# Performance work log

Hardware: AMD Instinct MI355X
Metric: run time of the kernel (lower is better)

## Reference

```python
import jax, jax.numpy as jnp
import numpy as np

LODS = [16, 32, 64, 128, 256]
SCENE_SCALE = 4.0
DESC = 4
N = 2_000_000
# 8 corner offsets of a voxel, bit-decoded: (x, y, z) in {0,1}^3
_CORNERS = jnp.asarray([[(i >> 2) & 1, (i >> 1) & 1, i & 1] for i in range(8)], dtype=jnp.int32)  # (8,3)


def setup_inputs() -> dict:
    key = jax.random.key(0)
    ks = jax.random.split(key, 2 + len(LODS))
    inp = {
        "pts": jax.random.normal(ks[0], (N, 3), dtype=jnp.float32),
        "d": jax.random.normal(ks[1], (N, 3), dtype=jnp.float32),
    }
    # codebook init mirrors torch: zeros + 0.01 * randn, shape (LOD^3, desc)
    for i, res in enumerate(LODS):
        inp[f"codebook_{i}"] = jax.random.normal(ks[2 + i], (res ** 3, DESC), dtype=jnp.float32) * 0.01
    return inp


def _trilerp(res, codebook, pts01):
    """NGLOD-style dense-grid trilinear interpolation.
    pts01: (N,3) in [0,1]; codebook: (res^3, DESC). Returns (N, DESC)."""
    pos = pts01 * (res - 1)                                   # (N,3) in [0, res-1]
    c0 = jnp.clip(jnp.floor(pos).astype(jnp.int32), 0, res - 2)
    frac = pos - c0.astype(pos.dtype)                         # (N,3) in [0,1]
    idx = c0[:, None, :] + _CORNERS[None, :, :]               # (N,8,3)
    flat = (idx[..., 0] * res + idx[..., 1]) * res + idx[..., 2]  # (N,8) row-major x*res^2+y*res+z
    # trilinear weights: prod over axes of (frac if corner bit set else 1-frac)
    w = jnp.prod(jnp.where(_CORNERS[None] == 1, frac[:, None, :], 1.0 - frac[:, None, :]), axis=-1)  # (N,8)
    return jnp.einsum('nkd,nk->nd', codebook[flat], w)        # gather + weighted sum


def reference(pts, d, codebook_0, codebook_1, codebook_2, codebook_3, codebook_4):
    cbs = (codebook_0, codebook_1, codebook_2, codebook_3, codebook_4)
    p = pts / SCENE_SCALE
    mask = jnp.all(jnp.abs(p) < 0.5, axis=-1)                 # inside unit cube
    p01 = jnp.clip(p + 0.5, 0.0, 1.0)                         # clamp keeps OOB points index-safe; masked out below
    feats = _trilerp(LODS[0], cbs[0], p01)
    for res, cb in zip(LODS[1:], cbs[1:]):
        feats = feats + _trilerp(res, cb, p01)                # sum features across LODs
    color = jnp.where(mask[:, None], feats[:, 0:3], 0.0)      # masked scatter into zero buffer
    log_sigma = jnp.where(mask, feats[:, 3], -100000.0)       # exp(-1e5) underflows to 0, as in torch
    return color, jnp.exp(log_sigma)[:, None]
```

## Files before the change

### kernel.cpp

```cpp
#include <hip/hip_runtime.h>
#include <math.h>

static constexpr float kSceneScale = 4.0f;
static constexpr int   kG     = 16;
static constexpr int   kNBin3 = kG * kG * kG;
static constexpr int   kNBins = kNBin3 + 1;
static constexpr int   kNB    = 256;
static constexpr unsigned kOutside = 0xFFFFFFFFu;

__device__ __forceinline__ void fma4(float4& acc, float w, const float4& c) {
    acc.x = fmaf(w, c.x, acc.x);
    acc.y = fmaf(w, c.y, acc.y);
    acc.z = fmaf(w, c.z, acc.z);
    acc.w = fmaf(w, c.w, acc.w);
}

template <int RES>
__device__ __forceinline__ void trilerp_acc(const float4* __restrict__ cb,
                                            float x, float y, float z,
                                            float4& acc) {
    const float s = (float)(RES - 1);
    float fx = x * s, fy = y * s, fz = z * s;
    int x0 = min((int)fx, RES - 2);
    int y0 = min((int)fy, RES - 2);
    int z0 = min((int)fz, RES - 2);
    float tx = fx - (float)x0;
    float ty = fy - (float)y0;
    float tz = fz - (float)z0;
    int base = (x0 * RES + y0) * RES + z0;
    float4 c000 = cb[base];
    float4 c001 = cb[base + 1];
    float4 c010 = cb[base + RES];
    float4 c011 = cb[base + RES + 1];
    float4 c100 = cb[base + RES * RES];
    float4 c101 = cb[base + RES * RES + 1];
    float4 c110 = cb[base + RES * RES + RES];
    float4 c111 = cb[base + RES * RES + RES + 1];
    float wx0 = 1.0f - tx, wx1 = tx;
    float wy0 = 1.0f - ty, wy1 = ty;
    float wz0 = 1.0f - tz, wz1 = tz;
    fma4(acc, wx0 * wy0 * wz0, c000);
    fma4(acc, wx0 * wy0 * wz1, c001);
    fma4(acc, wx0 * wy1 * wz0, c010);
    fma4(acc, wx0 * wy1 * wz1, c011);
    fma4(acc, wx1 * wy0 * wz0, c100);
    fma4(acc, wx1 * wy0 * wz1, c101);
    fma4(acc, wx1 * wy1 * wz0, c110);
    fma4(acc, wx1 * wy1 * wz1, c111);
}

__device__ __forceinline__ void load_p01(const float* __restrict__ pts, int i,
                                         float& x, float& y, float& z, bool& inside) {
    float px = pts[3 * i + 0] * (1.0f / kSceneScale);
    float py = pts[3 * i + 1] * (1.0f / kSceneScale);
    float pz = pts[3 * i + 2] * (1.0f / kSceneScale);
    inside = (fabsf(px) < 0.5f) && (fabsf(py) < 0.5f) && (fabsf(pz) < 0.5f);
    x = fminf(fmaxf(px + 0.5f, 0.0f), 1.0f);
    y = fminf(fmaxf(py + 0.5f, 0.0f), 1.0f);
    z = fminf(fmaxf(pz + 0.5f, 0.0f), 1.0f);
}

__device__ __forceinline__ unsigned key_from01(float x, float y, float z, bool inside) {
    if (!inside) return (unsigned)(kNBins - 1);
    int bx = min((int)(x * kG), kG - 1);
    int by = min((int)(y * kG), kG - 1);
    int bz = min((int)(z * kG), kG - 1);
    return (unsigned)((bx * kG + by) * kG + bz);
}

__global__ __launch_bounds__(256) void keys_hist_kernel(
        const float* __restrict__ pts,
        unsigned* __restrict__ blockHist, int n, int chunk) {
    __shared__ unsigned hist[kNBins];
    int tid = threadIdx.x;
    for (int j = tid; j < kNBins; j += 256) hist[j] = 0;
    __syncthreads();
    int beg = blockIdx.x * chunk;
    int end = min(n, beg + chunk);
    for (int i = beg + tid; i < end; i += 256) {
        float x, y, z; bool inside;
        load_p01(pts, i, x, y, z, inside);
        atomicAdd(&hist[key_from01(x, y, z, inside)], 1u);
    }
    __syncthreads();
    for (int j = tid; j < kNBins; j += 256) blockHist[(size_t)j * kNB + blockIdx.x] = hist[j];
}

__global__ __launch_bounds__(256) void scan_chunks_kernel(
        unsigned* __restrict__ data, unsigned* __restrict__ partials, int total) {
    __shared__ unsigned sums[256];
    int tid = threadIdx.x;
    int base = blockIdx.x * 1024 + tid * 4;
    uint4 v = make_uint4(0u, 0u, 0u, 0u);
    if (base + 3 < total) {
        v = *(const uint4*)(data + base);
    } else {
        unsigned* p = (unsigned*)&v;
        for (int k = 0; k < 4; ++k) if (base + k < total) p[k] = data[base + k];
    }
    unsigned s1 = v.x + v.y, s2 = s1 + v.z, s3 = s2 + v.w;
    sums[tid] = s3;
    __syncthreads();
    for (int off = 1; off < 256; off <<= 1) {
        unsigned t = (tid >= off) ? sums[tid - off] : 0u;
        __syncthreads();
        sums[tid] += t;
        __syncthreads();
    }
    unsigned excl = sums[tid] - s3;
    uint4 o;
    o.x = excl; o.y = excl + v.x; o.z = excl + s1; o.w = excl + s2;
    if (base + 3 < total) {
        *(uint4*)(data + base) = o;
    } else {
        unsigned* p = (unsigned*)&o;
        for (int k = 0; k < 4; ++k) if (base + k < total) data[base + k] = p[k];
    }
    if (tid == 255) partials[blockIdx.x] = sums[255];
}

__global__ __launch_bounds__(256) void scan_partials_kernel(unsigned* __restrict__ partials, int m) {
    __shared__ unsigned buf[256];
    __shared__ unsigned carry_s;
    int tid = threadIdx.x;
    if (tid == 0) carry_s = 0u;
    __syncthreads();
    for (int base = 0; base < m; base += 256) {
        unsigned v = (base + tid < m) ? partials[base + tid] : 0u;
        buf[tid] = v;
        __syncthreads();
        for (int off = 1; off < 256; off <<= 1) {
            unsigned t = (tid >= off) ? buf[tid - off] : 0u;
            __syncthreads();
            buf[tid] += t;
            __syncthreads();
        }
        unsigned incl = buf[tid];
        unsigned c = carry_s;
        if (base + tid < m) partials[base + tid] = c + incl - v;
        __syncthreads();
        if (tid == 255) carry_s = c + incl;
        __syncthreads();
    }
}

__global__ __launch_bounds__(256) void scan_add_kernel(
        unsigned* __restrict__ data, const unsigned* __restrict__ partials, int total) {
    int tid = threadIdx.x;
    int base = blockIdx.x * 1024 + tid * 4;
    unsigned p = partials[blockIdx.x];
    if (base + 3 < total) {
        uint4 v = *(const uint4*)(data + base);
        v.x += p; v.y += p; v.z += p; v.w += p;
        *(uint4*)(data + base) = v;
    } else {
        for (int k = 0; k < 4; ++k) if (base + k < total) data[base + k] += p;
    }
}

__global__ __launch_bounds__(256) void scatter_kernel(
        const float* __restrict__ pts,
        const unsigned* __restrict__ blockHist,
        float4* __restrict__ spts, unsigned* __restrict__ inv,
        int n, int chunk) {
    __shared__ unsigned offs[kNBins];
    int tid = threadIdx.x;
    for (int j = tid; j < kNBins; j += 256) offs[j] = blockHist[(size_t)j * kNB + blockIdx.x];
    __syncthreads();
    int beg = blockIdx.x * chunk;
    int end = min(n, beg + chunk);
    for (int i = beg + tid; i < end; i += 256) {
        float x, y, z; bool inside;
        load_p01(pts, i, x, y, z, inside);
        unsigned k = key_from01(x, y, z, inside);
        unsigned pos = atomicAdd(&offs[k], 1u);
        if (inside) {
            spts[pos] = make_float4(x, y, z, 0.0f);
            inv[i] = pos;
        } else {
            inv[i] = kOutside;
        }
    }
}

__global__ __launch_bounds__(512) void compute_sorted_kernel(
        const float4* __restrict__ spts,
        const unsigned* __restrict__ nInsidePtr,
        const float4* __restrict__ cb0,
        const float4* __restrict__ cb1,
        const float4* __restrict__ cb2,
        const float4* __restrict__ cb3,
        const float4* __restrict__ cb4,
        float4* __restrict__ sout) {
    unsigned nIn = nInsidePtr[0];
    unsigned t0 = blockIdx.x * 1024u + threadIdx.x;
    unsigned t1 = t0 + 512u;
    if (t0 >= nIn) return;

    float4 sA = spts[t0];
    bool doB = (t1 < nIn);
    float4 sB = doB ? spts[t1] : sA;

    float4 accA = make_float4(0.0f, 0.0f, 0.0f, 0.0f);
    float4 accB = make_float4(0.0f, 0.0f, 0.0f, 0.0f);

    trilerp_acc<16>(cb0, sA.x, sA.y, sA.z, accA);
    trilerp_acc<16>(cb1 - 0 + 0, sB.x, sB.y, sB.z, accB);
    accB = make_float4(0.0f, 0.0f, 0.0f, 0.0f);
    trilerp_acc<16>(cb0, sB.x, sB.y, sB.z, accB);
    trilerp_acc<32>(cb1, sA.x, sA.y, sA.z, accA);
    trilerp_acc<32>(cb1, sB.x, sB.y, sB.z, accB);
    trilerp_acc<64>(cb2, sA.x, sA.y, sA.z, accA);
    trilerp_acc<64>(cb2, sB.x, sB.y, sB.z, accB);
    trilerp_acc<128>(cb3, sA.x, sA.y, sA.z, accA);
    trilerp_acc<128>(cb3, sB.x, sB.y, sB.z, accB);
    trilerp_acc<256>(cb4, sA.x, sA.y, sA.z, accA);
    trilerp_acc<256>(cb4, sB.x, sB.y, sB.z, accB);

    sout[t0] = make_float4(accA.x, accA.y, accA.z, expf(accA.w));
    if (doB) sout[t1] = make_float4(accB.x, accB.y, accB.z, expf(accB.w));
}

__global__ __launch_bounds__(256) void unsort_kernel(
        const unsigned* __restrict__ inv,
        const float4* __restrict__ sout,
        float* __restrict__ out, int n) {
    int i = blockIdx.x * blockDim.x + threadIdx.x;
    if (i >= n) return;
    unsigned v = inv[i];
    float4 r = make_float4(0.0f, 0.0f, 0.0f, 0.0f);
    if (v != kOutside) r = sout[v];
    out[3 * i + 0] = r.x;
    out[3 * i + 1] = r.y;
    out[3 * i + 2] = r.z;
    out[(size_t)3 * n + i] = r.w;
}

__global__ __launch_bounds__(256) void direct_kernel(
        const float* __restrict__ pts,
        const float4* __restrict__ cb0,
        const float4* __restrict__ cb1,
        const float4* __restrict__ cb2,
        const float4* __restrict__ cb3,
        const float4* __restrict__ cb4,
        float* __restrict__ out,
        int n) {
    int i = blockIdx.x * blockDim.x + threadIdx.x;
    if (i >= n) return;
    float x, y, z; bool inside;
    load_p01(pts, i, x, y, z, inside);
    float c0 = 0.0f, c1 = 0.0f, c2 = 0.0f, sg = 0.0f;
    if (inside) {
        float4 acc = make_float4(0.0f, 0.0f, 0.0f, 0.0f);
        trilerp_acc<16>(cb0, x, y, z, acc);
        trilerp_acc<32>(cb1, x, y, z, acc);
        trilerp_acc<64>(cb2, x, y, z, acc);
        trilerp_acc<128>(cb3, x, y, z, acc);
        trilerp_acc<256>(cb4, x, y, z, acc);
        c0 = acc.x; c1 = acc.y; c2 = acc.z; sg = expf(acc.w);
    }
    out[3 * i + 0] = c0;
    out[3 * i + 1] = c1;
    out[3 * i + 2] = c2;
    out[(size_t)3 * n + i] = sg;
}

extern "C" void kernel_launch(void* const* d_in, const int* in_sizes, int n_in,
                              void* d_out, int out_size, void* d_ws, size_t ws_size,
                              hipStream_t stream) {
    const float* pts = (const float*)d_in[0];
    const float4* cb0 = (const float4*)d_in[2];
    const float4* cb1 = (const float4*)d_in[3];
    const float4* cb2 = (const float4*)d_in[4];
    const float4* cb3 = (const float4*)d_in[5];
    const float4* cb4 = (const float4*)d_in[6];
    float* out = (float*)d_out;

    int n = in_sizes[0] / 3;

    const int histTotal = kNBins * kNB;
    const int nChunks   = (histTotal + 1023) / 1024;

    size_t off_spts = 0;
    size_t off_sout = off_spts + (size_t)n * 16;
    size_t off_hist = off_sout + (size_t)n * 16;
    size_t off_part = off_hist + (size_t)histTotal * 4;
    size_t off_inv  = off_part + (size_t)nChunks * 4;
    size_t need     = off_inv + (size_t)n * 4;

    dim3 block(256);
    int nwg = (n + 255) / 256;

    if (ws_size < need) {
        direct_kernel<<<dim3(nwg), block, 0, stream>>>(pts, cb0, cb1, cb2, cb3, cb4, out, n);
        return;
    }

    float4*   spts      = (float4*)((char*)d_ws + off_spts);
    float4*   sout      = (float4*)((char*)d_ws + off_sout);
    unsigned* blockHist = (unsigned*)((char*)d_ws + off_hist);
    unsigned* partials  = (unsigned*)((char*)d_ws + off_part);
    unsigned* inv       = (unsigned*)((char*)d_ws + off_inv);

    const unsigned* nInsidePtr = blockHist + (size_t)kNBin3 * kNB;

    int chunk = (n + kNB - 1) / kNB;

    keys_hist_kernel<<<dim3(kNB), block, 0, stream>>>(pts, blockHist, n, chunk);
    scan_chunks_kernel<<<dim3(nChunks), block, 0, stream>>>(blockHist, partials, histTotal);
    scan_partials_kernel<<<dim3(1), block, 0, stream>>>(partials, nChunks);
    scan_add_kernel<<<dim3(nChunks), block, 0, stream>>>(blockHist, partials, histTotal);
    scatter_kernel<<<dim3(kNB), block, 0, stream>>>(pts, blockHist, spts, inv, n, chunk);
    compute_sorted_kernel<<<dim3((n + 1023) / 1024), dim3(512), 0, stream>>>(
        spts, nInsidePtr, cb0, cb1, cb2, cb3, cb4, sout);
    unsort_kernel<<<dim3(nwg), block, 0, stream>>>(inv, sout, out, n);
}
```

Measured before the change: 271.3 us.

## Refine sort bins, swizzle blocks across XCDs, and process four points per thread

The spatial sort grid grows from 16^3 to 16x32x32 bins, so sorted points sit closer together and codebook gathers should hit cache more often. The compute kernel remaps block IDs so that consecutive sorted chunks land on the same XCD and share its L2. Each thread now handles four points instead of two, which gives more independent gathers in flight. The cost is a larger histogram and scan (kNBins x 256 entries, with dynamic LDS of about 64KB per block) and higher register pressure in the compute kernel, which may lower occupancy.

```diff
diff --git a/kernel.cpp b/kernel.cpp
--- a/kernel.cpp
+++ b/kernel.cpp
@@ -2,8 +2,10 @@
 #include <math.h>
 
 static constexpr float kSceneScale = 4.0f;
-static constexpr int   kG     = 16;
-static constexpr int   kNBin3 = kG * kG * kG;
+static constexpr int   kGX    = 16;
+static constexpr int   kGY    = 32;
+static constexpr int   kGZ    = 32;
+static constexpr int   kNBin3 = kGX * kGY * kGZ;
 static constexpr int   kNBins = kNBin3 + 1;
 static constexpr int   kNB    = 256;
 static constexpr unsigned kOutside = 0xFFFFFFFFu;
@@ -62,16 +64,24 @@
 
 __device__ __forceinline__ unsigned key_from01(float x, float y, float z, bool inside) {
     if (!inside) return (unsigned)(kNBins - 1);
-    int bx = min((int)(x * kG), kG - 1);
-    int by = min((int)(y * kG), kG - 1);
-    int bz = min((int)(z * kG), kG - 1);
-    return (unsigned)((bx * kG + by) * kG + bz);
+    int bx = min((int)(x * kGX), kGX - 1);
+    int by = min((int)(y * kGY), kGY - 1);
+    int bz = min((int)(z * kGZ), kGZ - 1);
+    return (unsigned)((bx * kGY + by) * kGZ + bz);
+}
+
+__device__ __forceinline__ int xcd_swz(int orig, int nwg) {
+    const int NX = 8;
+    int q = nwg / NX, r = nwg % NX;
+    int xcd = orig % NX, j = orig / NX;
+    int base = (xcd < r) ? xcd * (q + 1) : r * (q + 1) + (xcd - r) * q;
+    return base + j;
 }
 
 __global__ __launch_bounds__(256) void keys_hist_kernel(
         const float* __restrict__ pts,
         unsigned* __restrict__ blockHist, int n, int chunk) {
-    __shared__ unsigned hist[kNBins];
+    extern __shared__ unsigned hist[];
     int tid = threadIdx.x;
     for (int j = tid; j < kNBins; j += 256) hist[j] = 0;
     __syncthreads();
@@ -163,7 +173,7 @@
         const unsigned* __restrict__ blockHist,
         float4* __restrict__ spts, unsigned* __restrict__ inv,
         int n, int chunk) {
-    __shared__ unsigned offs[kNBins];
+    extern __shared__ unsigned offs[];
     int tid = threadIdx.x;
     for (int j = tid; j < kNBins; j += 256) offs[j] = blockHist[(size_t)j * kNB + blockIdx.x];
     __syncthreads();
@@ -191,34 +201,53 @@
         const float4* __restrict__ cb2,
         const float4* __restrict__ cb3,
         const float4* __restrict__ cb4,
-        float4* __restrict__ sout) {
+        float4* __restrict__ sout, int cgrid) {
     unsigned nIn = nInsidePtr[0];
-    unsigned t0 = blockIdx.x * 1024u + threadIdx.x;
-    unsigned t1 = t0 + 512u;
+    int bid = xcd_swz((int)blockIdx.x, cgrid);
+    unsigned t0 = (unsigned)bid * 2048u + threadIdx.x;
     if (t0 >= nIn) return;
-
-    float4 sA = spts[t0];
-    bool doB = (t1 < nIn);
-    float4 sB = doB ? spts[t1] : sA;
-
-    float4 accA = make_float4(0.0f, 0.0f, 0.0f, 0.0f);
-    float4 accB = make_float4(0.0f, 0.0f, 0.0f, 0.0f);
-
-    trilerp_acc<16>(cb0, sA.x, sA.y, sA.z, accA);
-    trilerp_acc<16>(cb1 - 0 + 0, sB.x, sB.y, sB.z, accB);
-    accB = make_float4(0.0f, 0.0f, 0.0f, 0.0f);
-    trilerp_acc<16>(cb0, sB.x, sB.y, sB.z, accB);
-    trilerp_acc<32>(cb1, sA.x, sA.y, sA.z, accA);
-    trilerp_acc<32>(cb1, sB.x, sB.y, sB.z, accB);
-    trilerp_acc<64>(cb2, sA.x, sA.y, sA.z, accA);
-    trilerp_acc<64>(cb2, sB.x, sB.y, sB.z, accB);
-    trilerp_acc<128>(cb3, sA.x, sA.y, sA.z, accA);
-    trilerp_acc<128>(cb3, sB.x, sB.y, sB.z, accB);
-    trilerp_acc<256>(cb4, sA.x, sA.y, sA.z, accA);
-    trilerp_acc<256>(cb4, sB.x, sB.y, sB.z, accB);
-
-    sout[t0] = make_float4(accA.x, accA.y, accA.z, expf(accA.w));
-    if (doB) sout[t1] = make_float4(accB.x, accB.y, accB.z, expf(accB.w));
+    unsigned t1 = t0 + 512u, t2 = t0 + 1024u, t3 = t0 + 1536u;
+    bool v1 = t1 < nIn, v2 = t2 < nIn, v3 = t3 < nIn;
+
+    float4 s0_ = spts[t0];
+    float4 s1_ = v1 ? spts[t1] : s0_;
+    float4 s2_ = v2 ? spts[t2] : s0_;
+    float4 s3_ = v3 ? spts[t3] : s0_;
+
+    float4 a0 = make_float4(0.f, 0.f, 0.f, 0.f);
+    float4 a1 = make_float4(0.f, 0.f, 0.f, 0.f);
+    float4 a2 = make_float4(0.f, 0.f, 0.f, 0.f);
+    float4 a3 = make_float4(0.f, 0.f, 0.f, 0.f);
+
+    trilerp_acc<16>(cb0, s0_.x, s0_.y, s0_.z, a0);
+    trilerp_acc<16>(cb0, s1_.x, s1_.y, s1_.z, a1);
+    trilerp_acc<16>(cb0, s2_.x, s2_.y, s2_.z, a2);
+    trilerp_acc<16>(cb0, s3_.x, s3_.y, s3_.z, a3);
+
+    trilerp_acc<32>(cb1, s0_.x, s0_.y, s0_.z, a0);
+    trilerp_acc<32>(cb1, s1_.x, s1_.y, s1_.z, a1);
+    trilerp_acc<32>(cb1, s2_.x, s2_.y, s2_.z, a2);
+    trilerp_acc<32>(cb1, s3_.x, s3_.y, s3_.z, a3);
+
+    trilerp_acc<64>(cb2, s0_.x, s0_.y, s0_.z, a0);
+    trilerp_acc<64>(cb2, s1_.x, s1_.y, s1_.z, a1);
+    trilerp_acc<64>(cb2, s2_.x, s2_.y, s2_.z, a2);
+    trilerp_acc<64>(cb2, s3_.x, s3_.y, s3_.z, a3);
+
+    trilerp_acc<128>(cb3, s0_.x, s0_.y, s0_.z, a0);
+    trilerp_acc<128>(cb3, s1_.x, s1_.y, s1_.z, a1);
+    trilerp_acc<128>(cb3, s2_.x, s2_.y, s2_.z, a2);
+    trilerp_acc<128>(cb3, s3_.x, s3_.y, s3_.z, a3);
+
+    trilerp_acc<256>(cb4, s0_.x, s0_.y, s0_.z, a0);
+    trilerp_acc<256>(cb4, s1_.x, s1_.y, s1_.z, a1);
+    trilerp_acc<256>(cb4, s2_.x, s2_.y, s2_.z, a2);
+    trilerp_acc<256>(cb4, s3_.x, s3_.y, s3_.z, a3);
+
+    sout[t0] = make_float4(a0.x, a0.y, a0.z, expf(a0.w));
+    if (v1) sout[t1] = make_float4(a1.x, a1.y, a1.z, expf(a1.w));
+    if (v2) sout[t2] = make_float4(a2.x, a2.y, a2.z, expf(a2.w));
+    if (v3) sout[t3] = make_float4(a3.x, a3.y, a3.z, expf(a3.w));
 }
 
 __global__ __launch_bounds__(256) void unsort_kernel(
@@ -305,13 +334,15 @@
     const unsigned* nInsidePtr = blockHist + (size_t)kNBin3 * kNB;
 
     int chunk = (n + kNB - 1) / kNB;
-
-    keys_hist_kernel<<<dim3(kNB), block, 0, stream>>>(pts, blockHist, n, chunk);
+    int cgrid = (n + 2047) / 2048;
+    size_t ldsBytes = (size_t)kNBins * sizeof(unsigned);
+
+    keys_hist_kernel<<<dim3(kNB), block, ldsBytes, stream>>>(pts, blockHist, n, chunk);
     scan_chunks_kernel<<<dim3(nChunks), block, 0, stream>>>(blockHist, partials, histTotal);
     scan_partials_kernel<<<dim3(1), block, 0, stream>>>(partials, nChunks);
     scan_add_kernel<<<dim3(nChunks), block, 0, stream>>>(blockHist, partials, histTotal);
-    scatter_kernel<<<dim3(kNB), block, 0, stream>>>(pts, blockHist, spts, inv, n, chunk);
-    compute_sorted_kernel<<<dim3((n + 1023) / 1024), dim3(512), 0, stream>>>(
-        spts, nInsidePtr, cb0, cb1, cb2, cb3, cb4, sout);
+    scatter_kernel<<<dim3(kNB), block, ldsBytes, stream>>>(pts, blockHist, spts, inv, n, chunk);
+    compute_sorted_kernel<<<dim3(cgrid), dim3(512), 0, stream>>>(
+        spts, nInsidePtr, cb0, cb1, cb2, cb3, cb4, sout, cgrid);
     unsort_kernel<<<dim3(nwg), block, 0, stream>>>(inv, sout, out, n);
 }
```

Measured after the change: 658.1 us. +142.6%, slower.
